# Kernel tuning notes

Measured on AMD Instinct MI355X. Metric: run time of the kernel, lower is better.

The kernel has to match this reference:

```python
import jax, jax.numpy as jnp
import numpy as np
from jax import lax

B, C, H, W, D = 2, 64, 32, 32, 32
N = H * W * D          # input_size = 32768
P = 64                 # proj_size
NH = 4                 # num_heads
HD = C // NH           # head dim = 16
LN_EPS = 1e-5
BN_EPS = 1e-5


def setup_inputs() -> dict:
    key = jax.random.key(0)
    ks = jax.random.split(key, 10)
    s = lambda k, shape: (jax.random.normal(k, shape, jnp.float32) * 0.02)
    return dict(
        x=jax.random.normal(ks[0], (B, C, H, W, D), jnp.float32),
        ln_w=jnp.ones((C,), jnp.float32), ln_b=jnp.zeros((C,), jnp.float32),
        gamma=1e-6 * jnp.ones((C,), jnp.float32),
        temp1=jnp.ones((NH, 1, 1), jnp.float32),
        temp2=jnp.ones((NH, 1, 1), jnp.float32),
        W_qkvv=s(ks[1], (4 * C, C)),                      # Linear(C,4C), no bias
        W_EF=s(ks[2], (P, N)), b_EF=jnp.zeros((P,), jnp.float32),  # shared E=F
        W_o1=s(ks[3], (C // 2, C)), b_o1=jnp.zeros((C // 2,), jnp.float32),
        W_o2=s(ks[4], (C // 2, C)), b_o2=jnp.zeros((C // 2,), jnp.float32),
        conv1_w=s(ks[5], (C, C, 3, 3, 3)),
        conv2_w=s(ks[6], (C, C, 3, 3, 3)),
        bn1_w=jnp.ones((C,), jnp.float32), bn1_b=jnp.zeros((C,), jnp.float32),
        bn2_w=jnp.ones((C,), jnp.float32), bn2_b=jnp.zeros((C,), jnp.float32),
        conv8_w=s(ks[7], (C, C, 1, 1, 1)), conv8_b=jnp.zeros((C,), jnp.float32),
    )


def _ln(x, w, b):
    mu = jnp.mean(x, axis=-1, keepdims=True)
    var = jnp.mean(jnp.square(x - mu), axis=-1, keepdims=True)
    return (x - mu) * lax.rsqrt(var + LN_EPS) * w + b


def _l2norm(x):  # F.normalize(dim=-1), eps=1e-12
    n = jnp.sqrt(jnp.sum(jnp.square(x), axis=-1, keepdims=True))
    return x / jnp.maximum(n, 1e-12)


def _bn_eval(x, w, b):  # BatchNorm3d in eval mode, running mean 0 / var 1
    scale = (w * lax.rsqrt(jnp.float32(1.0 + BN_EPS))).reshape(1, -1, 1, 1, 1)
    return x * scale + b.reshape(1, -1, 1, 1, 1)


def _conv3d(x, w, pad):
    return lax.conv_general_dilated(
        x, w, window_strides=(1, 1, 1), padding=[(pad, pad)] * 3,
        dimension_numbers=('NCDHW', 'OIDHW', 'NCDHW'))


def _lrelu(x):
    return jnp.where(x >= 0, x, 0.01 * x)


def _epa(xn, W_qkvv, W_EF, b_EF, temp1, temp2, W_o1, b_o1, W_o2, b_o2):
    b, n, c = xn.shape
    qkvv = (xn @ W_qkvv.T).reshape(b, n, 4, NH, HD).transpose(2, 0, 3, 1, 4)  # [4,B,h,N,d]
    q, k, v_ca, v_sa = [jnp.swapaxes(qkvv[i], -2, -1) for i in range(4)]      # [B,h,d,N]
    # shared linear projection E = F over the token axis N -> P
    k_proj = jnp.einsum('bhdn,pn->bhdp', k, W_EF) + b_EF
    v_proj = jnp.einsum('bhdn,pn->bhdp', v_sa, W_EF) + b_EF
    qn, kn = _l2norm(q), _l2norm(k)
    # channel attention: [B,h,d,d]
    attn_ca = jax.nn.softmax(jnp.einsum('bhdn,bhen->bhde', qn, kn) * temp1, axis=-1)
    x_ca = jnp.einsum('bhde,bhen->bhdn', attn_ca, v_ca)                       # [B,h,d,N]
    x_ca = x_ca.transpose(0, 3, 1, 2).reshape(b, n, c)
    # spatial attention with projected K/V: [B,h,N,P]
    attn_sa = jax.nn.softmax(jnp.einsum('bhdn,bhdp->bhnp', qn, k_proj) * temp2, axis=-1)
    x_sa = jnp.einsum('bhnp,bhdp->bhnd', attn_sa, v_proj)                     # [B,h,N,d]
    # faithful to original UNETR++ code: permute(0,3,1,2) then reshape(B,N,C)
    x_sa = x_sa.transpose(0, 3, 1, 2).reshape(b, n, c)
    x_sa = x_sa @ W_o1.T + b_o1
    x_ca = x_ca @ W_o2.T + b_o2
    return jnp.concatenate([x_sa, x_ca], axis=-1)


def reference(x, ln_w, ln_b, gamma, temp1, temp2, W_qkvv, W_EF, b_EF,
              W_o1, b_o1, W_o2, b_o2, conv1_w, conv2_w,
              bn1_w, bn1_b, bn2_w, bn2_b, conv8_w, conv8_b):
    b, c, h, w, d = x.shape
    xs = x.reshape(b, c, h * w * d).transpose(0, 2, 1)  # [B,N,C]
    attn = xs + gamma * _epa(_ln(xs, ln_w, ln_b), W_qkvv, W_EF, b_EF,
                             temp1, temp2, W_o1, b_o1, W_o2, b_o2)
    attn_skip = attn.reshape(b, h, w, d, c).transpose(0, 4, 1, 2, 3)  # [B,C,H,W,D]
    # UnetResBlock (stride 1, in==out -> identity residual), BN in eval mode
    out = _lrelu(_bn_eval(_conv3d(attn_skip, conv1_w, 1), bn1_w, bn1_b))
    out = _bn_eval(_conv3d(out, conv2_w, 1), bn2_w, bn2_b)
    out = _lrelu(out + attn_skip)
    # conv8: Dropout3d (off, eval) + 1x1x1 conv with bias
    y = _conv3d(out, conv8_w, 0) + conv8_b.reshape(1, -1, 1, 1, 1)
    return attn_skip + y
```

## Files before the change

kernel.cpp:

```cpp
#include <hip/hip_runtime.h>

#define NTOK 32768

typedef __attribute__((ext_vector_type(8))) short short8;
typedef __attribute__((ext_vector_type(4))) short short4_t;
typedef __attribute__((ext_vector_type(4))) float f32x4;

__device__ __forceinline__ short f2b(float f) {
    union { float f; unsigned u; } v; v.f = f;
    unsigned r = v.u + 0x7fffu + ((v.u >> 16) & 1u);
    return (short)(r >> 16);
}
__device__ __forceinline__ float b2f(short s) {
    union { float f; unsigned u; } v;
    v.u = ((unsigned)(unsigned short)s) << 16;
    return v.f;
}

__global__ void k_repack(const float* __restrict__ w1, const float* __restrict__ w2,
                         const float* __restrict__ w8, const float* __restrict__ wef,
                         const float* __restrict__ wq, const float* __restrict__ bEF,
                         short* __restrict__ wb1, short* __restrict__ wb2,
                         short* __restrict__ wb8, short* __restrict__ wefb,
                         short* __restrict__ wqb, float* __restrict__ kp,
                         float* __restrict__ vp, float* __restrict__ qd)
{
    int i = blockIdx.x * 256 + threadIdx.x;
    if (i >= 2349312) return;
    if (i >= 2347008) { qd[i - 2347008] = 0.f; return; }
    if (i >= 2338816) {
        int j = i - 2338816;
        float v = bEF[j & 63];
        kp[j] = v; vp[j] = v; return;
    }
    if (i >= 2322432) { int j = i - 2322432; wqb[j] = f2b(wq[j]); return; }
    if (i >= 225280)  { int j = i - 225280;  wefb[j] = f2b(wef[j]); return; }
    if (i >= 221184)  { int j = i - 221184;  wb8[j] = f2b(w8[j]); return; }
    int sel = i >= 110592;
    int j = sel ? i - 110592 : i;
    int tap = j >> 12;
    int r = j & 4095;
    int oc = r >> 6, ic = r & 63;
    const float* w = sel ? w2 : w1;
    short* o = sel ? wb2 : wb1;
    o[j] = f2b(w[(oc * 64 + ic) * 27 + tap]);
}

__global__ __launch_bounds__(256) void k_ln_qkvv(
    const float* __restrict__ x, const float* __restrict__ lnw,
    const float* __restrict__ lnb, const short* __restrict__ wqb,
    short* __restrict__ qkvvb)
{
    __shared__ __align__(16) short Wl[256 * 72];
    __shared__ __align__(16) short tr[256 * 72];
    __shared__ float red1[4][64], red2[4][64];
    __shared__ float mu_s[64], rs_s[64];
    short* al = tr;

    int bid = blockIdx.x;
    int b = bid >> 9;
    int n0 = (bid & 511) << 6;
    int tid = threadIdx.x;

    for (int i = tid; i < 2048; i += 256) {
        int out = i >> 3, q8 = (i & 7) * 8;
        *(short8*)&Wl[out * 72 + q8] = *(const short8*)&wqb[out * 64 + q8];
    }

    int t = tid & 63, cq = tid >> 6;
    float xr[16];
    float s1 = 0.f, s2 = 0.f;
    const float* xb = x + (((size_t)(b * 64 + cq * 16)) << 15) + n0 + t;
#pragma unroll
    for (int j = 0; j < 16; ++j) {
        float v = xb[(size_t)j << 15];
        xr[j] = v; s1 += v; s2 += v * v;
    }
    red1[cq][t] = s1; red2[cq][t] = s2;
    __syncthreads();
    if (tid < 64) {
        float a = red1[0][tid] + red1[1][tid] + red1[2][tid] + red1[3][tid];
        float q = red2[0][tid] + red2[1][tid] + red2[2][tid] + red2[3][tid];
        float mu = a * (1.f / 64.f);
        float var = q * (1.f / 64.f) - mu * mu;
        mu_s[tid] = mu;
        rs_s[tid] = rsqrtf(var + 1e-5f);
    }
    __syncthreads();
    {
        float mu = mu_s[t], rs = rs_s[t];
        short8 p0, p1;
#pragma unroll
        for (int j = 0; j < 8; ++j) {
            int c = cq * 16 + j;
            p0[j] = f2b((xr[j] - mu) * rs * lnw[c] + lnb[c]);
        }
#pragma unroll
        for (int j = 0; j < 8; ++j) {
            int c = cq * 16 + 8 + j;
            p1[j] = f2b((xr[8 + j] - mu) * rs * lnw[c] + lnb[c]);
        }
        *(short8*)&al[t * 72 + cq * 16] = p0;
        *(short8*)&al[t * 72 + cq * 16 + 8] = p1;
    }
    __syncthreads();

    int w = tid >> 6, lane = tid & 63, l15 = lane & 15, quad = lane >> 4;
    f32x4 acc[4][4];
#pragma unroll
    for (int mt = 0; mt < 4; ++mt)
#pragma unroll
        for (int nt = 0; nt < 4; ++nt) acc[mt][nt] = (f32x4){0.f, 0.f, 0.f, 0.f};
#pragma unroll
    for (int ks = 0; ks < 2; ++ks) {
        short8 af[4], bf[4];
#pragma unroll
        for (int mt = 0; mt < 4; ++mt)
            af[mt] = *(const short8*)&al[(mt * 16 + l15) * 72 + quad * 8 + ks * 32];
#pragma unroll
        for (int nt = 0; nt < 4; ++nt)
            bf[nt] = *(const short8*)&Wl[(w * 64 + nt * 16 + l15) * 72 + quad * 8 + ks * 32];
#pragma unroll
        for (int mt = 0; mt < 4; ++mt)
#pragma unroll
            for (int nt = 0; nt < 4; ++nt)
                acc[mt][nt] = __builtin_amdgcn_mfma_f32_16x16x32_bf16(af[mt], bf[nt], acc[mt][nt], 0, 0, 0);
    }
    __syncthreads();

#pragma unroll
    for (int mt = 0; mt < 4; ++mt)
#pragma unroll
        for (int nt = 0; nt < 4; ++nt) {
            int out = w * 64 + nt * 16 + l15;
            short4_t sv;
#pragma unroll
            for (int r = 0; r < 4; ++r) sv[r] = f2b(acc[mt][nt][r]);
            *(short4_t*)&tr[out * 72 + mt * 16 + quad * 4] = sv;
        }
    __syncthreads();
    for (int i = tid; i < 2048; i += 256) {
        int o = i >> 3, tq = (i & 7) * 8;
        short8 v = *(const short8*)&tr[o * 72 + tq];
        int isel = o >> 6, h = (o >> 4) & 3, d = o & 15;
        *(short8*)&qkvvb[((size_t)(((isel * 2 + b) * 4 + h) * 16 + d) << 15) + n0 + tq] = v;
    }
}

__global__ __launch_bounds__(256) void k_pq(
    const short* __restrict__ qkvvb, const short* __restrict__ wefb,
    float* __restrict__ kp, float* __restrict__ vp, float* __restrict__ qd,
    float* __restrict__ qn_acc, float* __restrict__ kn_acc)
{
    __shared__ float redb[3][64][38];
    int kc = blockIdx.x, bh = blockIdx.y;
    int tid = threadIdx.x;
    int w = tid >> 6, lane = tid & 63, l15 = lane & 15, quad = lane >> 4;
    size_t qrow = ((size_t)(bh * 16 + l15)) << 15;
    size_t krow = ((size_t)(128 + bh * 16 + l15)) << 15;
    size_t vrow = ((size_t)(384 + bh * 16 + l15)) << 15;
    int nbase = kc * 1024 + w * 256 + quad * 8;
    f32x4 acck[4], accv[4], accqd, accqq, acckk;
#pragma unroll
    for (int nt = 0; nt < 4; ++nt) {
        acck[nt] = (f32x4){0.f, 0.f, 0.f, 0.f};
        accv[nt] = (f32x4){0.f, 0.f, 0.f, 0.f};
    }
    accqd = (f32x4){0.f, 0.f, 0.f, 0.f};
    accqq = (f32x4){0.f, 0.f, 0.f, 0.f};
    acckk = (f32x4){0.f, 0.f, 0.f, 0.f};
#pragma unroll
    for (int ks = 0; ks < 8; ++ks) {
        int n = nbase + ks * 32;
        short8 qf = *(const short8*)&qkvvb[qrow + n];
        short8 kf = *(const short8*)&qkvvb[krow + n];
        short8 vf = *(const short8*)&qkvvb[vrow + n];
        accqd = __builtin_amdgcn_mfma_f32_16x16x32_bf16(qf, kf, accqd, 0, 0, 0);
        accqq = __builtin_amdgcn_mfma_f32_16x16x32_bf16(qf, qf, accqq, 0, 0, 0);
        acckk = __builtin_amdgcn_mfma_f32_16x16x32_bf16(kf, kf, acckk, 0, 0, 0);
#pragma unroll
        for (int nt = 0; nt < 4; ++nt) {
            short8 wf = *(const short8*)&wefb[(((size_t)(nt * 16 + l15)) << 15) + n];
            acck[nt] = __builtin_amdgcn_mfma_f32_16x16x32_bf16(kf, wf, acck[nt], 0, 0, 0);
            accv[nt] = __builtin_amdgcn_mfma_f32_16x16x32_bf16(vf, wf, accv[nt], 0, 0, 0);
        }
    }
    int diag = (quad == (l15 >> 2));
    float qqv = diag ? accqq[l15 & 3] : 0.f;
    float kkv = diag ? acckk[l15 & 3] : 0.f;
    if (w > 0) {
        float* p = &redb[w - 1][lane][0];
#pragma unroll
        for (int nt = 0; nt < 4; ++nt)
#pragma unroll
            for (int r = 0; r < 4; ++r) { p[nt * 4 + r] = acck[nt][r]; p[16 + nt * 4 + r] = accv[nt][r]; }
#pragma unroll
        for (int r = 0; r < 4; ++r) p[32 + r] = accqd[r];
        p[36] = qqv; p[37] = kkv;
    }
    __syncthreads();
    if (w == 0) {
#pragma unroll
        for (int wv = 0; wv < 3; ++wv) {
            const float* p = &redb[wv][lane][0];
#pragma unroll
            for (int nt = 0; nt < 4; ++nt)
#pragma unroll
                for (int r = 0; r < 4; ++r) { acck[nt][r] += p[nt * 4 + r]; accv[nt][r] += p[16 + nt * 4 + r]; }
#pragma unroll
            for (int r = 0; r < 4; ++r) accqd[r] += p[32 + r];
            qqv += p[36]; kkv += p[37];
        }
        int d = quad * 4;
#pragma unroll
        for (int nt = 0; nt < 4; ++nt)
#pragma unroll
            for (int r = 0; r < 4; ++r) {
                int idx = (bh * 16 + d + r) * 64 + nt * 16 + l15;
                atomicAdd(&kp[idx], acck[nt][r]);
                atomicAdd(&vp[idx], accv[nt][r]);
            }
#pragma unroll
        for (int r = 0; r < 4; ++r)
            atomicAdd(&qd[bh * 256 + (d + r) * 16 + l15], accqd[r]);
        if (diag) {
            atomicAdd(&qn_acc[bh * 16 + l15], qqv);
            atomicAdd(&kn_acc[bh * 16 + l15], kkv);
        }
    }
}

__global__ void k_softmax_ca(const float* __restrict__ qd,
    const float* __restrict__ qn_acc, const float* __restrict__ kn_acc,
    const float* __restrict__ temp1, float* __restrict__ attn,
    float* __restrict__ iqn, float* __restrict__ ikn)
{
    __shared__ float iqs[128], iks[128];
    int tid = threadIdx.x;
    if (tid < 128) {
        float v = 1.f / fmaxf(sqrtf(qn_acc[tid]), 1e-12f);
        iqs[tid] = v; iqn[tid] = v;
    } else {
        int j = tid - 128;
        float v = 1.f / fmaxf(sqrtf(kn_acc[j]), 1e-12f);
        iks[j] = v; ikn[j] = v;
    }
    __syncthreads();
    int r = tid;
    if (r >= 128) return;
    int bh = r >> 4;
    int h = bh & 3;
    float iq = iqs[r];
    float t1 = temp1[h];
    float sc[16];
    float mx = -1e30f;
#pragma unroll
    for (int e = 0; e < 16; ++e) {
        float v = qd[r * 16 + e] * iq * iks[bh * 16 + e] * t1;
        sc[e] = v; mx = fmaxf(mx, v);
    }
    float s = 0.f;
#pragma unroll
    for (int e = 0; e < 16; ++e) { sc[e] = __expf(sc[e] - mx); s += sc[e]; }
    float inv = 1.f / s;
#pragma unroll
    for (int e = 0; e < 16; ++e) attn[r * 16 + e] = sc[e] * inv;
}

__global__ __launch_bounds__(256) void k_attn(
    const short* __restrict__ qkvvb, const float* __restrict__ inv_qn,
    const float* __restrict__ kp, const float* __restrict__ vp,
    const float* __restrict__ temp2, const float* __restrict__ a_ca,
    short* __restrict__ xsab, short* __restrict__ xcab)
{
    __shared__ float kl[16][64];
    __shared__ float vl[16][64];
    __shared__ float alca[16][16];
    __shared__ float iq[16];
    int bh = blockIdx.y; int b = bh >> 2, h = bh & 3;
    int tid = threadIdx.x;
    for (int i = tid; i < 1024; i += 256) {
        kl[i >> 6][i & 63] = kp[bh * 1024 + i];
        vl[i >> 6][i & 63] = vp[bh * 1024 + i];
    }
    alca[tid >> 4][tid & 15] = a_ca[bh * 256 + tid];
    if (tid < 16) iq[tid] = inv_qn[bh * 16 + tid];
    __syncthreads();
    int n = blockIdx.x * 256 + tid;

    {
        const short* vbase = qkvvb + (((size_t)(256 + bh * 16)) << 15) + n;
        float acc[16];
#pragma unroll
        for (int d = 0; d < 16; ++d) acc[d] = 0.f;
#pragma unroll
        for (int e = 0; e < 16; ++e) {
            float va = b2f(vbase[(size_t)e << 15]);
#pragma unroll
            for (int d = 0; d < 16; ++d) acc[d] += alca[d][e] * va;
        }
        short8 lo, hi;
#pragma unroll
        for (int j = 0; j < 8; ++j) { lo[j] = f2b(acc[j]); hi[j] = f2b(acc[j + 8]); }
        short* op = xcab + ((size_t)(b * NTOK + n)) * 64 + h * 16;
        *(short8*)&op[0] = lo;
        *(short8*)&op[8] = hi;
    }

    const short* qbase = qkvvb + (((size_t)(bh * 16)) << 15) + n;
    float qn_[16];
#pragma unroll
    for (int d = 0; d < 16; ++d) qn_[d] = b2f(qbase[(size_t)d << 15]) * iq[d];
    float t2 = temp2[h];
    float sc[64];
#pragma unroll
    for (int p = 0; p < 64; ++p) sc[p] = 0.f;
#pragma unroll
    for (int d = 0; d < 16; ++d) {
        float qv = qn_[d];
        const float4* kr = (const float4*)&kl[d][0];
#pragma unroll
        for (int p4 = 0; p4 < 16; ++p4) {
            float4 kv = kr[p4];
            sc[p4 * 4 + 0] += qv * kv.x; sc[p4 * 4 + 1] += qv * kv.y;
            sc[p4 * 4 + 2] += qv * kv.z; sc[p4 * 4 + 3] += qv * kv.w;
        }
    }
    float mx = -1e30f;
#pragma unroll
    for (int p = 0; p < 64; ++p) { sc[p] *= t2; mx = fmaxf(mx, sc[p]); }
    float s = 0.f;
#pragma unroll
    for (int p = 0; p < 64; ++p) { sc[p] = __expf(sc[p] - mx); s += sc[p]; }
    float inv = 1.f / s;
#pragma unroll
    for (int p = 0; p < 64; ++p) sc[p] *= inv;
    short* ob = xsab + (size_t)b * 2097152 + n;
#pragma unroll
    for (int d = 0; d < 16; ++d) {
        const float4* vr = (const float4*)&vl[d][0];
        float a0 = 0, a1 = 0, a2 = 0, a3 = 0;
#pragma unroll
        for (int p4 = 0; p4 < 16; ++p4) {
            float4 vv = vr[p4];
            a0 += sc[p4 * 4] * vv.x; a1 += sc[p4 * 4 + 1] * vv.y;
            a2 += sc[p4 * 4 + 2] * vv.z; a3 += sc[p4 * 4 + 3] * vv.w;
        }
        ob[(size_t)(d * 4 + h) << 15] = f2b((a0 + a1) + (a2 + a3));
    }
}

__global__ __launch_bounds__(256) void k_epilogue(
    const float* __restrict__ x, const short* __restrict__ xsab,
    const short* __restrict__ xcab, const float* __restrict__ Wo1,
    const float* __restrict__ bo1, const float* __restrict__ Wo2,
    const float* __restrict__ bo2, const float* __restrict__ gamma,
    float* __restrict__ attn_skip, short* __restrict__ gA)
{
    __shared__ float W1[32][64];
    __shared__ float W2[32][64];
    int tid = threadIdx.x;
    for (int i = tid; i < 2048; i += 256) {
        W1[i >> 6][i & 63] = Wo1[i];
        W2[i >> 6][i & 63] = Wo2[i];
    }
    __syncthreads();
    int bid = blockIdx.x;
    int b = bid >> 9;
    int n0 = (bid & 511) << 6;
    int t = tid & 63, cg = tid >> 6;
    int n = n0 + t;
    const short* row = (cg < 2) ? xsab + (size_t)b * 2097152 + (size_t)n * 64
                                : xcab + ((size_t)(b * NTOK + n)) * 64;
    const float* Wb = (cg < 2) ? &W1[(cg & 1) * 16][0] : &W2[(cg & 1) * 16][0];
    const float* bias = (cg < 2) ? bo1 + (cg & 1) * 16 : bo2 + (cg & 1) * 16;
    float acc[16];
#pragma unroll
    for (int j = 0; j < 16; ++j) acc[j] = 0.f;
#pragma unroll
    for (int c8 = 0; c8 < 8; ++c8) {
        short8 rv8 = *(const short8*)&row[c8 * 8];
        float rv[8];
#pragma unroll
        for (int q = 0; q < 8; ++q) rv[q] = b2f(rv8[q]);
#pragma unroll
        for (int j = 0; j < 16; ++j) {
            const float* wr = &Wb[j * 64 + c8 * 8];
#pragma unroll
            for (int q = 0; q < 8; ++q) acc[j] += rv[q] * wr[q];
        }
    }
    float vals[16];
#pragma unroll
    for (int j = 0; j < 16; ++j) {
        int c = cg * 16 + j;
        size_t idx = (((size_t)(b * 64 + c)) << 15) + n;
        float v = x[idx] + gamma[c] * (acc[j] + bias[j]);
        attn_skip[idx] = v;
        vals[j] = v;
    }
    short8 lo, hi;
#pragma unroll
    for (int j = 0; j < 8; ++j) { lo[j] = f2b(vals[j]); hi[j] = f2b(vals[j + 8]); }
    short* gp = gA + ((size_t)(b * NTOK + n)) * 64 + cg * 16;
    *(short8*)&gp[0] = lo;
    *(short8*)&gp[8] = hi;
}

template <int MODE>
__global__ __launch_bounds__(256) void k_conv3m(
    const short* __restrict__ gin, const short* __restrict__ wb,
    const float* __restrict__ bnw, const float* __restrict__ bnb,
    const float* __restrict__ skip, short* __restrict__ goutS,
    const short* __restrict__ wb8, const float* __restrict__ b8,
    float* __restrict__ io)
{
    __shared__ __align__(16) short inl_s[24480];
    __shared__ __align__(16) short wl_s[5120];
    __shared__ __align__(16) short a2_s[MODE ? 9216 : 16];
    int bx = blockIdx.x;
    int bb = bx >> 8;
    int z0 = (bx >> 3) & 31;
    int y0 = (bx & 7) * 4;
    int tid = threadIdx.x;
    int lane = tid & 63, wv = tid >> 6;
    int l15 = lane & 15, quad = lane >> 4;
    int wo = tid >> 2, wq = tid & 3;

    f32x4 acc[2][4];
#pragma unroll
    for (int s = 0; s < 2; ++s)
#pragma unroll
        for (int nt = 0; nt < 4; ++nt) acc[s][nt] = (f32x4){0.f, 0.f, 0.f, 0.f};

    int boff[4];
#pragma unroll
    for (int nt = 0; nt < 4; ++nt) boff[nt] = (nt * 16 + l15) * 40 + quad * 8;

    for (int chunk = 0; chunk < 2; ++chunk) {
        __syncthreads();
        for (int i = tid; i < 2448; i += 256) {
            int p = i >> 2, icq = i & 3;
            int xi = p % 34; int t2 = p / 34; int yi = t2 % 6; int zi = t2 / 6;
            int gz = z0 + zi - 1, gy = y0 + yi - 1, gx = xi - 1;
            short8 v = {0, 0, 0, 0, 0, 0, 0, 0};
            if ((unsigned)gz < 32u && (unsigned)gy < 32u && (unsigned)gx < 32u)
                v = *(const short8*)&gin[((size_t)(bb * NTOK + gz * 1024 + gy * 32 + gx)) * 64 + chunk * 32 + icq * 8];
            *(short8*)&inl_s[p * 40 + icq * 8] = v;
        }
        short8 wreg = *(const short8*)&wb[(size_t)wo * 64 + chunk * 32 + wq * 8];
        for (int tap = 0; tap < 27; ++tap) {
            *(short8*)&wl_s[(tap & 1) * 2560 + wo * 40 + wq * 8] = wreg;
            if (tap < 26)
                wreg = *(const short8*)&wb[(size_t)((tap + 1) * 64 + wo) * 64 + chunk * 32 + wq * 8];
            __syncthreads();
            int kz = tap / 9, ky = (tap / 3) % 3, kx = tap % 3;
            const short* wlb = &wl_s[(tap & 1) * 2560];
            short8 bf[4];
#pragma unroll
            for (int nt = 0; nt < 4; ++nt) bf[nt] = *(const short8*)&wlb[boff[nt]];
            int rowb = (kz * 6 + wv + ky) * 34;
#pragma unroll
            for (int s = 0; s < 2; ++s) {
                short8 af = *(const short8*)&inl_s[(rowb + s * 16 + l15 + kx) * 40 + quad * 8];
#pragma unroll
                for (int nt = 0; nt < 4; ++nt)
                    acc[s][nt] = __builtin_amdgcn_mfma_f32_16x16x32_bf16(af, bf[nt], acc[s][nt], 0, 0, 0);
            }
        }
    }
    __syncthreads();
    float rb = rsqrtf(1.f + 1e-5f);
    if (MODE == 0) {
        short* outS = inl_s;
#pragma unroll
        for (int nt = 0; nt < 4; ++nt) {
            int oc = nt * 16 + l15;
            float sc_ = bnw[oc] * rb, sh_ = bnb[oc];
#pragma unroll
            for (int s = 0; s < 2; ++s) {
                f32x4 v = acc[s][nt];
#pragma unroll
                for (int r = 0; r < 4; ++r) {
                    int pos = wv * 32 + s * 16 + quad * 4 + r;
                    float val = v[r] * sc_ + sh_;
                    val = val >= 0.f ? val : 0.01f * val;
                    outS[pos * 72 + oc] = f2b(val);
                }
            }
        }
        __syncthreads();
        for (int i = tid; i < 1024; i += 256) {
            int p = i >> 3, cq = i & 7;
            short8 v = *(const short8*)&outS[p * 72 + cq * 8];
            int y = p >> 5, x = p & 31;
            *(short8*)&goutS[((size_t)(bb * NTOK + z0 * 1024 + (y0 + y) * 32 + x)) * 64 + cq * 8] = v;
        }
    } else {
        float* outF = (float*)inl_s;
#pragma unroll
        for (int nt = 0; nt < 4; ++nt) {
            int oc = nt * 16 + l15;
#pragma unroll
            for (int s = 0; s < 2; ++s) {
                f32x4 v = acc[s][nt];
#pragma unroll
                for (int r = 0; r < 4; ++r) {
                    int pos = wv * 32 + s * 16 + quad * 4 + r;
                    outF[oc * 132 + pos] = v[r];
                }
            }
        }
        __syncthreads();
        f32x4 skr[8];
#pragma unroll
        for (int it = 0; it < 8; ++it) {
            int i = it * 256 + tid;
            int oc = i >> 5, xq = i & 31, pos0 = xq * 4;
            f32x4 c4 = *(const f32x4*)&outF[oc * 132 + pos0];
            int y = pos0 >> 5, xx = pos0 & 31;
            size_t g = (((size_t)(bb * 64 + oc)) << 15) + ((z0 * 32 + (y0 + y)) * 32 + xx);
            f32x4 sk = *(const f32x4*)&skip[g];
            skr[it] = sk;
            float sc_ = bnw[oc] * rb, sh_ = bnb[oc];
#pragma unroll
            for (int r = 0; r < 4; ++r) {
                float val = c4[r] * sc_ + sh_ + sk[r];
                val = val >= 0.f ? val : 0.01f * val;
                a2_s[(pos0 + r) * 72 + oc] = f2b(val);
            }
        }
        for (int i = tid; i < 512; i += 256) {
            int ocw = i >> 3, cq = i & 7;
            *(short8*)&wl_s[ocw * 80 + cq * 8] = *(const short8*)&wb8[ocw * 64 + cq * 8];
        }
        __syncthreads();
        f32x4 acc2[2][4];
#pragma unroll
        for (int s = 0; s < 2; ++s)
#pragma unroll
            for (int nt = 0; nt < 4; ++nt) acc2[s][nt] = (f32x4){0.f, 0.f, 0.f, 0.f};
#pragma unroll
        for (int ks = 0; ks < 2; ++ks) {
            short8 a8[2], b8f[4];
#pragma unroll
            for (int s = 0; s < 2; ++s)
                a8[s] = *(const short8*)&a2_s[(wv * 32 + s * 16 + l15) * 72 + quad * 8 + ks * 32];
#pragma unroll
            for (int nt = 0; nt < 4; ++nt)
                b8f[nt] = *(const short8*)&wl_s[(nt * 16 + l15) * 80 + quad * 8 + ks * 32];
#pragma unroll
            for (int s = 0; s < 2; ++s)
#pragma unroll
                for (int nt = 0; nt < 4; ++nt)
                    acc2[s][nt] = __builtin_amdgcn_mfma_f32_16x16x32_bf16(a8[s], b8f[nt], acc2[s][nt], 0, 0, 0);
        }
        __syncthreads();
#pragma unroll
        for (int nt = 0; nt < 4; ++nt) {
            int oc = nt * 16 + l15;
#pragma unroll
            for (int s = 0; s < 2; ++s) {
                f32x4 v = acc2[s][nt];
#pragma unroll
                for (int r = 0; r < 4; ++r) {
                    int pos = wv * 32 + s * 16 + quad * 4 + r;
                    outF[oc * 132 + pos] = v[r];
                }
            }
        }
        __syncthreads();
#pragma unroll
        for (int it = 0; it < 8; ++it) {
            int i = it * 256 + tid;
            int oc = i >> 5, xq = i & 31, pos0 = xq * 4;
            f32x4 cv = *(const f32x4*)&outF[oc * 132 + pos0];
            int y = pos0 >> 5, xx = pos0 & 31;
            size_t g = (((size_t)(bb * 64 + oc)) << 15) + ((z0 * 32 + (y0 + y)) * 32 + xx);
            float bias8 = b8[oc];
            f32x4 o;
#pragma unroll
            for (int r = 0; r < 4; ++r) o[r] = skr[it][r] + cv[r] + bias8;
            *(f32x4*)&io[g] = o;
        }
    }
}

extern "C" void kernel_launch(void* const* d_in, const int* in_sizes, int n_in,
                              void* d_out, int out_size, void* d_ws, size_t ws_size,
                              hipStream_t stream) {
    const float* x      = (const float*)d_in[0];
    const float* ln_w   = (const float*)d_in[1];
    const float* ln_b   = (const float*)d_in[2];
    const float* gamma  = (const float*)d_in[3];
    const float* temp1  = (const float*)d_in[4];
    const float* temp2  = (const float*)d_in[5];
    const float* W_qkvv = (const float*)d_in[6];
    const float* W_EF   = (const float*)d_in[7];
    const float* b_EF   = (const float*)d_in[8];
    const float* W_o1   = (const float*)d_in[9];
    const float* b_o1   = (const float*)d_in[10];
    const float* W_o2   = (const float*)d_in[11];
    const float* b_o2   = (const float*)d_in[12];
    const float* conv1w = (const float*)d_in[13];
    const float* conv2w = (const float*)d_in[14];
    const float* bn1_w  = (const float*)d_in[15];
    const float* bn1_b  = (const float*)d_in[16];
    const float* bn2_w  = (const float*)d_in[17];
    const float* bn2_b  = (const float*)d_in[18];
    const float* conv8w = (const float*)d_in[19];
    const float* conv8b = (const float*)d_in[20];

    short* qkvvb = (short*)d_ws;
    float* kp    = (float*)(qkvvb + 16777216);
    float* vp    = kp + 8192;
    float* qd    = vp + 8192;
    float* qn_acc= qd + 2048;
    float* kn_acc= qn_acc + 128;
    float* a_ca  = kn_acc + 128;
    float* iqn   = a_ca + 2048;
    float* ikn   = iqn + 128;
    short* xcab  = (short*)(ikn + 128);
    short* xsab  = xcab + 4194304;
    short* gA    = xsab + 4194304;
    short* g1    = gA + 4194304;
    short* wb1   = g1 + 4194304;
    short* wb2   = wb1 + 110592;
    short* wb8   = wb2 + 110592;
    short* wefb  = wb8 + 4096;
    short* wqb   = wefb + 2097152;

    float* attn_skip = (float*)d_out;

    hipLaunchKernelGGL(k_repack, dim3(9177), dim3(256), 0, stream,
                       conv1w, conv2w, conv8w, W_EF, W_qkvv, b_EF,
                       wb1, wb2, wb8, wefb, wqb, kp, vp, qd);
    hipLaunchKernelGGL(k_ln_qkvv, dim3(1024), dim3(256), 0, stream,
                       x, ln_w, ln_b, wqb, qkvvb);
    hipLaunchKernelGGL(k_pq, dim3(32, 8), dim3(256), 0, stream,
                       qkvvb, wefb, kp, vp, qd, qn_acc, kn_acc);
    hipLaunchKernelGGL(k_softmax_ca, dim3(1), dim3(256), 0, stream,
                       qd, qn_acc, kn_acc, temp1, a_ca, iqn, ikn);
    hipLaunchKernelGGL(k_attn, dim3(128, 8), dim3(256), 0, stream,
                       qkvvb, iqn, kp, vp, temp2, a_ca, xsab, xcab);
    hipLaunchKernelGGL(k_epilogue, dim3(1024), dim3(256), 0, stream,
                       x, xsab, xcab, W_o1, b_o1, W_o2, b_o2, gamma, attn_skip, gA);
    hipLaunchKernelGGL((k_conv3m<0>), dim3(512), dim3(256), 0, stream,
                       gA, wb1, bn1_w, bn1_b, (const float*)nullptr, g1,
                       (const short*)nullptr, (const float*)nullptr, (float*)nullptr);
    hipLaunchKernelGGL((k_conv3m<1>), dim3(512), dim3(256), 0, stream,
                       g1, wb2, bn2_w, bn2_b, attn_skip, (short*)nullptr,
                       wb8, conv8b, attn_skip);
}
```

Baseline: 256.6 us.

## Compute epilogue output projections with bf16 MFMA and stage gA through LDS

Replaces the scalar FP32 output-projection GEMMs in the epilogue kernel with bf16 MFMA 16x16x32 instructions. Each block now handles 256 tokens instead of 64, so the grid shrinks from 1024 to 256 blocks. The bf16 copy of attn_skip is transposed through padded shared memory so the gA writes are coalesced 16-byte stores. Weights are now rounded to bf16, which slightly changes numerics, and the smaller grid may lower occupancy on a GPU with many CUs.

```diff
diff --git a/kernel.cpp b/kernel.cpp
--- a/kernel.cpp
+++ b/kernel.cpp
@@ -357,54 +357,84 @@
     const float* __restrict__ bo2, const float* __restrict__ gamma,
     float* __restrict__ attn_skip, short* __restrict__ gA)
 {
-    __shared__ float W1[32][64];
-    __shared__ float W2[32][64];
+    __shared__ __align__(16) short Wl[64 * 72];
+    __shared__ __align__(16) short trS[256 * 72];
     int tid = threadIdx.x;
+    int bidx = blockIdx.x;
+    int b = bidx >> 7;
+    int n0 = (bidx & 127) << 8;
+    for (int i = tid; i < 4096; i += 256) {
+        int row = i >> 6, c = i & 63;
+        float wv = (row < 32) ? Wo1[row * 64 + c] : Wo2[(row - 32) * 64 + c];
+        Wl[row * 72 + c] = f2b(wv);
+    }
+    __syncthreads();
+
+    int w = tid >> 6, lane = tid & 63, l15 = lane & 15, quad = lane >> 4;
+    int tw = n0 + w * 64;
+    const short* sa_base = xsab + (size_t)b * 2097152;
+    const short* ca_base = xcab + (size_t)b * 2097152;
+
+    f32x4 acc_sa[4][2], acc_ca[4][2];
+#pragma unroll
+    for (int mt = 0; mt < 4; ++mt)
+#pragma unroll
+        for (int nt = 0; nt < 2; ++nt) {
+            acc_sa[mt][nt] = (f32x4){0.f, 0.f, 0.f, 0.f};
+            acc_ca[mt][nt] = (f32x4){0.f, 0.f, 0.f, 0.f};
+        }
+#pragma unroll
+    for (int ks = 0; ks < 2; ++ks) {
+        int ko = quad * 8 + ks * 32;
+        short8 b1[2], b2[2];
+#pragma unroll
+        for (int nt = 0; nt < 2; ++nt) {
+            b1[nt] = *(const short8*)&Wl[(nt * 16 + l15) * 72 + ko];
+            b2[nt] = *(const short8*)&Wl[(32 + nt * 16 + l15) * 72 + ko];
+        }
+#pragma unroll
+        for (int mt = 0; mt < 4; ++mt) {
+            int trow = tw + mt * 16 + l15;
+            short8 a1 = *(const short8*)&sa_base[(size_t)trow * 64 + ko];
+            short8 a2 = *(const short8*)&ca_base[(size_t)trow * 64 + ko];
+#pragma unroll
+            for (int nt = 0; nt < 2; ++nt) {
+                acc_sa[mt][nt] = __builtin_amdgcn_mfma_f32_16x16x32_bf16(a1, b1[nt], acc_sa[mt][nt], 0, 0, 0);
+                acc_ca[mt][nt] = __builtin_amdgcn_mfma_f32_16x16x32_bf16(a2, b2[nt], acc_ca[mt][nt], 0, 0, 0);
+            }
+        }
+    }
+
+#pragma unroll
+    for (int half = 0; half < 2; ++half) {
+#pragma unroll
+        for (int nt = 0; nt < 2; ++nt) {
+            int c = half * 32 + nt * 16 + l15;
+            float g = gamma[c];
+            float bias = half ? bo2[c - 32] : bo1[c];
+#pragma unroll
+            for (int mt = 0; mt < 4; ++mt) {
+                f32x4 a = half ? acc_ca[mt][nt] : acc_sa[mt][nt];
+                int tbase = tw + mt * 16 + quad * 4;
+                size_t gidx = (((size_t)(b * 64 + c)) << 15) + tbase;
+                f32x4 xv = *(const f32x4*)&x[gidx];
+                f32x4 o;
+#pragma unroll
+                for (int r = 0; r < 4; ++r) {
+                    float v = xv[r] + g * (a[r] + bias);
+                    o[r] = v;
+                    trS[(w * 64 + mt * 16 + quad * 4 + r) * 72 + c] = f2b(v);
+                }
+                *(f32x4*)&attn_skip[gidx] = o;
+            }
+        }
+    }
+    __syncthreads();
     for (int i = tid; i < 2048; i += 256) {
-        W1[i >> 6][i & 63] = Wo1[i];
-        W2[i >> 6][i & 63] = Wo2[i];
-    }
-    __syncthreads();
-    int bid = blockIdx.x;
-    int b = bid >> 9;
-    int n0 = (bid & 511) << 6;
-    int t = tid & 63, cg = tid >> 6;
-    int n = n0 + t;
-    const short* row = (cg < 2) ? xsab + (size_t)b * 2097152 + (size_t)n * 64
-                                : xcab + ((size_t)(b * NTOK + n)) * 64;
-    const float* Wb = (cg < 2) ? &W1[(cg & 1) * 16][0] : &W2[(cg & 1) * 16][0];
-    const float* bias = (cg < 2) ? bo1 + (cg & 1) * 16 : bo2 + (cg & 1) * 16;
-    float acc[16];
-#pragma unroll
-    for (int j = 0; j < 16; ++j) acc[j] = 0.f;
-#pragma unroll
-    for (int c8 = 0; c8 < 8; ++c8) {
-        short8 rv8 = *(const short8*)&row[c8 * 8];
-        float rv[8];
-#pragma unroll
-        for (int q = 0; q < 8; ++q) rv[q] = b2f(rv8[q]);
-#pragma unroll
-        for (int j = 0; j < 16; ++j) {
-            const float* wr = &Wb[j * 64 + c8 * 8];
-#pragma unroll
-            for (int q = 0; q < 8; ++q) acc[j] += rv[q] * wr[q];
-        }
-    }
-    float vals[16];
-#pragma unroll
-    for (int j = 0; j < 16; ++j) {
-        int c = cg * 16 + j;
-        size_t idx = (((size_t)(b * 64 + c)) << 15) + n;
-        float v = x[idx] + gamma[c] * (acc[j] + bias[j]);
-        attn_skip[idx] = v;
-        vals[j] = v;
-    }
-    short8 lo, hi;
-#pragma unroll
-    for (int j = 0; j < 8; ++j) { lo[j] = f2b(vals[j]); hi[j] = f2b(vals[j + 8]); }
-    short* gp = gA + ((size_t)(b * NTOK + n)) * 64 + cg * 16;
-    *(short8*)&gp[0] = lo;
-    *(short8*)&gp[8] = hi;
+        int tok = i >> 3, cq = (i & 7) * 8;
+        short8 v = *(const short8*)&trS[tok * 72 + cq];
+        *(short8*)&gA[((size_t)(b * NTOK + n0 + tok)) * 64 + cq] = v;
+    }
 }
 
 template <int MODE>
@@ -643,7 +673,7 @@
                        qd, qn_acc, kn_acc, temp1, a_ca, iqn, ikn);
     hipLaunchKernelGGL(k_attn, dim3(128, 8), dim3(256), 0, stream,
                        qkvvb, iqn, kp, vp, temp2, a_ca, xsab, xcab);
-    hipLaunchKernelGGL(k_epilogue, dim3(1024), dim3(256), 0, stream,
+    hipLaunchKernelGGL(k_epilogue, dim3(256), dim3(256), 0, stream,
                        x, xsab, xcab, W_o1, b_o1, W_o2, b_o2, gamma, attn_skip, gA);
     hipLaunchKernelGGL((k_conv3m<0>), dim3(512), dim3(256), 0, stream,
                        gA, wb1, bn1_w, bn1_b, (const float*)nullptr, g1,
```

After: 229.5 us. 10.5% less time.
